# Optimization experiments

Hardware: AMD Instinct MI355X
Metric: run time of the kernel (lower is better)

## Reference

```python
import jax, jax.numpy as jnp
import numpy as np

B, S, D, NH = 8, 2048, 1024, 8
HD = D // NH          # 128 head dim
UP = 2752             # round_up(2.6667*1024, 64) gated FFN up dim
EPS = 1e-6


def setup_inputs() -> dict:
    key = jax.random.key(0)
    ks = jax.random.split(key, 10)
    s_hd = 1.0 / np.sqrt(HD)
    s_d = 1.0 / np.sqrt(D)
    s_up = 1.0 / np.sqrt(UP)
    return {
        "x": jax.random.normal(ks[0], (B, S, D), jnp.float32),
        "rms1_w": 1.0 + 0.1 * jax.random.normal(ks[1], (D,), jnp.float32),
        "rms2_w": 1.0 + 0.1 * jax.random.normal(ks[2], (D,), jnp.float32),
        # block-diagonal per-head input projections for the 4 gates (i,f,z,o)
        "Wg": jax.random.normal(ks[3], (4, NH, HD, HD), jnp.float32) * s_hd,
        # block-diagonal per-head recurrent weights for the 4 gates
        "R": jax.random.normal(ks[4], (4, NH, HD, HD), jnp.float32) * s_hd,
        "b": jax.random.normal(ks[5], (4, D), jnp.float32) * 0.1,
        "gn_w": 1.0 + 0.1 * jax.random.normal(ks[6], (D,), jnp.float32),
        "W_gate": jax.random.normal(ks[7], (D, UP), jnp.float32) * s_d,
        "W_up": jax.random.normal(ks[8], (D, UP), jnp.float32) * s_d,
        "W_down": jax.random.normal(ks[9], (UP, D), jnp.float32) * s_up,
    }


def _rmsnorm(x, w):
    xf = x.astype(jnp.float32)
    return xf * jax.lax.rsqrt(jnp.mean(xf * xf, axis=-1, keepdims=True) + EPS) * w


def _slstm_block(x, rms1_w, rms2_w, Wg, R, b, gn_w, W_gate, W_up, W_down):
    # --- norm + sLSTM layer ---
    xn = _rmsnorm(x, rms1_w)                     # [B,S,D]
    xh = xn.reshape(B, S, NH, HD)
    # precompute input-side gate preactivations for all timesteps: [S,B,4,NH,HD]
    gx = jnp.einsum('bsni,gnoi->sbgno', xh, Wg) + b.reshape(4, NH, HD)

    zeros = jnp.zeros((B, NH, HD), jnp.float32)
    init = (zeros, zeros, zeros, zeros)          # h, c, n, m

    def step(carry, g):
        h, c, n, m = carry
        pre = g + jnp.einsum('bni,gnoi->bgno', h, R)   # [B,4,NH,HD]
        ir, fr, zr, o_r = pre[:, 0], pre[:, 1], pre[:, 2], pre[:, 3]
        logfplusm = m + jax.nn.log_sigmoid(fr)
        mnew = jnp.maximum(ir, logfplusm)
        i = jnp.exp(ir - mnew)
        f = jnp.exp(logfplusm - mnew)
        cnew = f * c + i * jnp.tanh(zr)
        nnew = f * n + i
        hnew = jax.nn.sigmoid(o_r) * cnew / nnew
        return (hnew, cnew, nnew, mnew), hnew

    (hl, cl, nl, ml), hs = jax.lax.scan(step, init, gx)
    hs = jnp.transpose(hs, (1, 0, 2, 3))         # [B,S,NH,HD]
    # per-head group norm (zero-mean layernorm within each head), weight only
    mu = jnp.mean(hs, axis=-1, keepdims=True)
    var = jnp.var(hs, axis=-1, keepdims=True)
    y = ((hs - mu) * jax.lax.rsqrt(var + EPS)).reshape(B, S, D) * gn_w
    x = x + y                                    # residual
    # --- norm + gated SiLU FFN ---
    xn2 = _rmsnorm(x, rms2_w)
    ff = (jax.nn.silu(xn2 @ W_gate) * (xn2 @ W_up)) @ W_down
    out = x + ff
    state = jnp.stack([hl, cl, nl, ml])          # [4,B,NH,HD] last (h,c,n,m)
    return out, state


def reference(x, rms1_w, rms2_w, Wg, R, b, gn_w, W_gate, W_up, W_down):
    return _slstm_block(x, rms1_w, rms2_w, Wg, R, b, gn_w, W_gate, W_up, W_down)
```

## Files before the change

### kernel.cpp

```cpp
#include <hip/hip_runtime.h>

typedef __bf16 bf16;
typedef bf16 bf16x8 __attribute__((ext_vector_type(8)));
typedef bf16 bf16x4 __attribute__((ext_vector_type(4)));
typedef float f32x4 __attribute__((ext_vector_type(4)));

#define B_ 8
#define S_ 2048
#define D_ 1024
#define NH_ 8
#define HD_ 128
#define UPP 2816
#define ROWS (B_*S_)

__device__ __forceinline__ void gload_lds16(const void* gsrc, void* ldsdst) {
  __builtin_amdgcn_global_load_lds(
      (const __attribute__((address_space(1))) void*)gsrc,
      (__attribute__((address_space(3))) void*)ldsdst, 16, 0, 0);
}

__global__ __launch_bounds__(256) void pack_wgr_kernel(
    const float* __restrict__ Wg, const float* __restrict__ R, const float* __restrict__ bv,
    bf16* __restrict__ Wgpk, bf16* __restrict__ Rpk, float* __restrict__ biaspk)
{
  const float K2 = 1.442695040888963f;
  int idx = blockIdx.x * 256 + threadIdx.x;
  if (idx < 8*512*128) {
    int k = idx & 127, j = (idx >> 7) & 511, n = idx >> 16;
    int g = (j >> 4) & 3, o = ((j >> 6) << 4) | (j & 15);
    float sc = (g == 2) ? 2.f*K2 : K2;
    size_t src = (((size_t)(g*8 + n)*128 + o)*128 + k);
    Wgpk[idx] = (bf16)(Wg[src] * sc);
    Rpk[idx]  = (bf16)(R[src] * sc);
  }
  if (idx < 8*512) {
    int j = idx & 511, n = idx >> 9;
    int g = (j >> 4) & 3, o = ((j >> 6) << 4) | (j & 15);
    float sc = (g == 2) ? 2.f*K2 : K2;
    biaspk[idx] = bv[g*1024 + n*128 + o] * sc;
  }
}

__global__ __launch_bounds__(256) void packT_kernel(
    const float* __restrict__ in, bf16* __restrict__ out,
    int K_out, int N_out, int K_in, int N_in)
{
  __shared__ float tile[64][65];
  int k0 = blockIdx.x * 64, j0 = blockIdx.y * 64;
  int tj = threadIdx.x & 63, t4 = threadIdx.x >> 6;
  #pragma unroll
  for (int p = 0; p < 16; ++p) {
    int kk = p*4 + t4, k = k0 + kk, j = j0 + tj;
    tile[kk][tj] = (k < K_in && j < N_in) ? in[(size_t)k * N_in + j] : 0.f;
  }
  __syncthreads();
  #pragma unroll
  for (int p = 0; p < 16; ++p) {
    int jj = p*4 + t4, j = j0 + jj, k = k0 + tj;
    if (j < N_out && k < K_out) out[(size_t)j * K_out + k] = (bf16)tile[tj][jj];
  }
}

__global__ __launch_bounds__(256) void rmsnorm1_kernel(
    const float* __restrict__ x, const float* __restrict__ w, bf16* __restrict__ xn)
{
  const int row = blockIdx.x, t = threadIdx.x;
  const size_t base = (size_t)row * D_;
  float4 xv = ((const float4*)(x + base))[t];
  float p = xv.x*xv.x + xv.y*xv.y + xv.z*xv.z + xv.w*xv.w;
  #pragma unroll
  for (int m = 1; m <= 32; m <<= 1) p += __shfl_xor(p, m);
  __shared__ float red[4];
  if ((t & 63) == 0) red[t >> 6] = p;
  __syncthreads();
  float rs = rsqrtf((red[0]+red[1]+red[2]+red[3]) * (1.f/1024.f) + 1e-6f);
  float4 wv = ((const float4*)w)[t];
  bf16x4 o;
  o[0] = (bf16)(xv.x*rs*wv.x); o[1] = (bf16)(xv.y*rs*wv.y);
  o[2] = (bf16)(xv.z*rs*wv.z); o[3] = (bf16)(xv.w*rs*wv.w);
  ((bf16x4*)(xn + base))[t] = o;
}

#define BM 128
#define BN 128
#define BKK 64
template<int MODE>
__global__ __launch_bounds__(256) void gemm_bt(
    const bf16* __restrict__ A, int lda,
    const bf16* __restrict__ B, int ldb,
    float* Cf, bf16* Cb, int ldc,
    const float* __restrict__ bias, const float* res, const bf16* gatein, int K)
{
  __shared__ __align__(16) bf16 As[BM*BKK];
  __shared__ __align__(16) bf16 Bs[BN*BKK];
  if constexpr (MODE == 0) {
    const int h = blockIdx.z;
    A += h * HD_;
    B += (size_t)h * (512*128);
    Cb += (size_t)h * ((size_t)ROWS * 512);
    bias += h * 512;
  }
  const int tid = threadIdx.x;
  const int lane = tid & 63, wave = tid >> 6;
  const int row0 = blockIdx.y * BM, col0 = blockIdx.x * BN;
  const int srow = lane >> 3, scol = (lane & 7) * 8;
  const int wr = (wave >> 1) * 64, wc = (wave & 1) * 64;
  const int fr = lane & 15, fg = lane >> 4;
  f32x4 acc[4][4] = {};

  for (int k0 = 0; k0 < K; k0 += BKK) {
    __syncthreads();
    #pragma unroll
    for (int c = 0; c < 4; ++c) {
      const int slot = wave * 4 + c;
      const int r = slot * 8 + srow;
      gload_lds16(A + (size_t)(row0 + r) * lda + (k0 + scol), &As[slot * 512]);
      gload_lds16(B + (size_t)(col0 + r) * ldb + (k0 + scol), &Bs[slot * 512]);
    }
    __syncthreads();
    #pragma unroll
    for (int kk = 0; kk < 2; ++kk) {
      bf16x8 af[4], bfv[4];
      #pragma unroll
      for (int m = 0; m < 4; ++m)
        af[m] = *(const bf16x8*)&As[(wr + m*16 + fr)*BKK + kk*32 + fg*8];
      #pragma unroll
      for (int nn = 0; nn < 4; ++nn)
        bfv[nn] = *(const bf16x8*)&Bs[(wc + nn*16 + fr)*BKK + kk*32 + fg*8];
      #pragma unroll
      for (int m = 0; m < 4; ++m)
        #pragma unroll
        for (int nn = 0; nn < 4; ++nn)
          acc[m][nn] = __builtin_amdgcn_mfma_f32_16x16x32_bf16(af[m], bfv[nn], acc[m][nn], 0, 0, 0);
    }
  }

  #pragma unroll
  for (int m = 0; m < 4; ++m) {
    const int rbase = row0 + wr + m*16 + fg*4;
    #pragma unroll
    for (int nn = 0; nn < 4; ++nn) {
      const int col = col0 + wc + nn*16 + fr;
      #pragma unroll
      for (int j = 0; j < 4; ++j) {
        const size_t off = (size_t)(rbase + j) * ldc + col;
        float v = acc[m][nn][j];
        if constexpr (MODE == 0) Cb[off] = (bf16)(v + bias[col]);
        if constexpr (MODE == 1) Cb[off] = (bf16)v;
        if constexpr (MODE == 2) Cf[off] = v + res[off];
        if constexpr (MODE == 3) {
          float gf = (float)gatein[off];
          Cb[off] = (bf16)(gf / (1.f + __expf(-gf)) * v);
        }
      }
    }
  }
}

__global__ __launch_bounds__(512, 1) void recur_kernel(
    const bf16* __restrict__ gx, const bf16* __restrict__ Rpk,
    bf16* __restrict__ hs, float* __restrict__ stateOut)
{
  const int n  = blockIdx.x >> 2;
  const int bp = blockIdx.x & 3;
  const int tid = threadIdx.x, w = tid >> 6, l = tid & 63;
  const int b16 = l & 15, fg = l >> 4;
  const int bl  = l & 1;
  const int r16 = (l >> 1) & 15;
  const int b   = bp*2 + bl;
  const int o   = w*16 + r16;
  const bool act = (l < 32);

  __shared__ __align__(16) bf16 H[2][2][136];
  __shared__ __align__(16) float scr[8][4][2][17];
  for (int i = tid; i < 2*2*136; i += 512) ((bf16*)H)[i] = (bf16)0.f;
  __syncthreads();

  bf16x8 rf[4][4];
  #pragma unroll
  for (int g = 0; g < 4; ++g)
    #pragma unroll
    for (int kk = 0; kk < 4; ++kk)
      rf[g][kk] = *(const bf16x8*)&Rpk[(size_t)n*65536 + (size_t)(w*64 + g*16 + b16)*128 + kk*32 + fg*8];

  f32x4 zv = {0.f, 0.f, 0.f, 0.f};
  asm volatile("" : "+v"(zv));

  float cS = 0.f, nS = 0.f, mS = 0.f, hv = 0.f;

  const bf16* gxp = gx + (size_t)n * ROWS * 512 + (size_t)b * S_ * 512
                    + (size_t)w * 64 + r16;
  bf16* hsp = hs + (size_t)b * S_ * D_ + n * HD_ + o;

  bf16 ga[4][4];
  #pragma unroll
  for (int g = 0; g < 4; ++g) {
    ga[0][g] = gxp[(size_t)0*512 + g*16];
    ga[1][g] = gxp[(size_t)1*512 + g*16];
  }

  auto step = [&](const bf16 (&Hr)[2][136], bf16 (&Hw)[2][136], int s,
                  bf16 (&gU)[4], bf16 (&gF)[4]) {
    bf16x8 hf[4];
    #pragma unroll
    for (int kk = 0; kk < 4; ++kk)
      hf[kk] = *(const bf16x8*)&Hr[b16 & 1][kk*32 + fg*8];

    {
      int sf = (s + 2 < S_) ? s + 2 : 0;
      #pragma unroll
      for (int g = 0; g < 4; ++g)
        gF[g] = gxp[(size_t)sf*512 + g*16];
    }

    f32x4 acc[4];
    #pragma unroll
    for (int g = 0; g < 4; ++g)
      acc[g] = __builtin_amdgcn_mfma_f32_16x16x32_bf16(rf[g][0], hf[0], zv, 0, 0, 0);
    #pragma unroll
    for (int kk = 1; kk < 4; ++kk)
      #pragma unroll
      for (int g = 0; g < 4; ++g)
        acc[g] = __builtin_amdgcn_mfma_f32_16x16x32_bf16(rf[g][kk], hf[kk], acc[g], 0, 0, 0);

    if (b16 < 2) {
      #pragma unroll
      for (int g = 0; g < 4; ++g)
        *(f32x4*)&scr[w][g][b16][fg*4] = acc[g];
    }
    float pre[4];
    #pragma unroll
    for (int g = 0; g < 4; ++g)
      pre[g] = scr[w][g][bl][r16];

    float ir  = pre[0] + (float)gU[0];
    float fr_ = pre[1] + (float)gU[1];
    float zr  = pre[2] + (float)gU[2];
    float og  = pre[3] + (float)gU[3];
    float t   = __builtin_amdgcn_exp2f(-fr_);
    float lfm = mS - __builtin_amdgcn_logf(1.f + t);
    float d   = ir - lfm;
    float e   = __builtin_amdgcn_exp2f(-fabsf(d));
    float iG  = (d >= 0.f) ? 1.f : e;
    float fG  = (d >= 0.f) ? e : 1.f;
    mS = fmaxf(ir, lfm);
    float e2  = __builtin_amdgcn_exp2f(zr);
    float th  = 1.f - 2.f*__builtin_amdgcn_rcpf(e2 + 1.f);
    cS = fG*cS + iG*th;
    nS = fG*nS + iG;
    float eo  = __builtin_amdgcn_exp2f(-og);
    hv = cS * __builtin_amdgcn_rcpf(nS + nS*eo);

    bf16 hb = (bf16)hv;
    if (act) {
      Hw[bl][o] = hb;
      hsp[(size_t)s*D_] = hb;
    }

    __builtin_amdgcn_sched_barrier(0);
    __builtin_amdgcn_s_waitcnt(0xC07F);
    __builtin_amdgcn_s_barrier();
    __builtin_amdgcn_sched_barrier(0);
  };

  for (int s = 0; s < S_; s += 4) {
    step(H[0], H[1], s,     ga[0], ga[2]);
    step(H[1], H[0], s + 1, ga[1], ga[3]);
    step(H[0], H[1], s + 2, ga[2], ga[0]);
    step(H[1], H[0], s + 3, ga[3], ga[1]);
  }

  if (act) {
    const float LN2 = 0.6931471805599453f;
    size_t sb = ((size_t)b*NH_ + n)*HD_ + o;
    stateOut[sb]         = hv;
    stateOut[8192  + sb] = cS;
    stateOut[16384 + sb] = nS;
    stateOut[24576 + sb] = mS * LN2;
  }
}

__global__ __launch_bounds__(256) void fuse_gn_kernel(
    const bf16* __restrict__ hs, const float* __restrict__ x,
    const float* __restrict__ gnw, const float* __restrict__ r2w,
    float* __restrict__ xr, bf16* __restrict__ xn2)
{
  const int row = blockIdx.x, t = threadIdx.x;
  const size_t base = (size_t)row * D_;
  bf16x4 hraw = ((const bf16x4*)(hs + base))[t];
  float h0 = (float)hraw[0], h1 = (float)hraw[1], h2 = (float)hraw[2], h3 = (float)hraw[3];
  float4 xv = ((const float4*)(x + base))[t];
  float sum = h0 + h1 + h2 + h3;
  float sq  = h0*h0 + h1*h1 + h2*h2 + h3*h3;
  #pragma unroll
  for (int m = 1; m <= 16; m <<= 1) { sum += __shfl_xor(sum, m); sq += __shfl_xor(sq, m); }
  float mu = sum * (1.f/128.f);
  float var = sq * (1.f/128.f) - mu*mu;
  float rstd = rsqrtf(var + 1e-6f);
  float4 gw = ((const float4*)gnw)[t];
  float r0 = xv.x + (h0-mu)*rstd*gw.x;
  float r1 = xv.y + (h1-mu)*rstd*gw.y;
  float r2 = xv.z + (h2-mu)*rstd*gw.z;
  float r3 = xv.w + (h3-mu)*rstd*gw.w;
  ((float4*)(xr + base))[t] = make_float4(r0, r1, r2, r3);
  float p = r0*r0 + r1*r1 + r2*r2 + r3*r3;
  #pragma unroll
  for (int m = 1; m <= 32; m <<= 1) p += __shfl_xor(p, m);
  __shared__ float red[4];
  if ((t & 63) == 0) red[t >> 6] = p;
  __syncthreads();
  float rs = rsqrtf((red[0]+red[1]+red[2]+red[3]) * (1.f/1024.f) + 1e-6f);
  float4 w2 = ((const float4*)r2w)[t];
  bf16x4 o;
  o[0] = (bf16)(r0*rs*w2.x); o[1] = (bf16)(r1*rs*w2.y);
  o[2] = (bf16)(r2*rs*w2.z); o[3] = (bf16)(r3*rs*w2.w);
  ((bf16x4*)(xn2 + base))[t] = o;
}

extern "C" void kernel_launch(void* const* d_in, const int* in_sizes, int n_in,
                              void* d_out, int out_size, void* d_ws, size_t ws_size,
                              hipStream_t stream)
{
  const float* x     = (const float*)d_in[0];
  const float* rms1w = (const float*)d_in[1];
  const float* rms2w = (const float*)d_in[2];
  const float* Wg    = (const float*)d_in[3];
  const float* R     = (const float*)d_in[4];
  const float* bvec  = (const float*)d_in[5];
  const float* gnw   = (const float*)d_in[6];
  const float* Wgate = (const float*)d_in[7];
  const float* Wup   = (const float*)d_in[8];
  const float* Wdown = (const float*)d_in[9];
  float* out = (float*)d_out;
  float* stateOut = out + (size_t)ROWS * D_;

  char* ws = (char*)d_ws;
  size_t off = 0;
  auto alloc = [&](size_t bytes) -> void* {
    void* p = ws + off; off += (bytes + 255) & ~(size_t)255; return p;
  };
  bf16*  xn     = (bf16*)alloc((size_t)ROWS * D_ * 2);
  bf16*  hsbuf  = (bf16*)alloc((size_t)ROWS * D_ * 2);
  bf16*  bigbuf = (bf16*)alloc((size_t)NH_ * ROWS * 512 * 2);
  bf16*  Wgpk   = (bf16*)alloc(8*512*128*2);
  bf16*  Rpk    = (bf16*)alloc(8*512*128*2);
  float* biaspk = (float*)alloc(8*512*4);
  bf16*  Wgatepk = (bf16*)alloc((size_t)UPP * D_ * 2);
  bf16*  Wuppk   = (bf16*)alloc((size_t)UPP * D_ * 2);
  bf16*  Wdownpk = (bf16*)alloc((size_t)D_ * UPP * 2);

  pack_wgr_kernel<<<2048, 256, 0, stream>>>(Wg, R, bvec, Wgpk, Rpk, biaspk);
  packT_kernel<<<dim3(16, 44), 256, 0, stream>>>(Wgate, Wgatepk, 1024, 2816, 1024, 2752);
  packT_kernel<<<dim3(16, 44), 256, 0, stream>>>(Wup,   Wuppk,   1024, 2816, 1024, 2752);
  packT_kernel<<<dim3(44, 16), 256, 0, stream>>>(Wdown, Wdownpk, 2816, 1024, 2752, 1024);

  rmsnorm1_kernel<<<ROWS, 256, 0, stream>>>(x, rms1w, xn);

  gemm_bt<0><<<dim3(4, 128, 8), 256, 0, stream>>>(xn, D_, Wgpk, 128,
      nullptr, bigbuf, 512, biaspk, nullptr, nullptr, 128);

  recur_kernel<<<32, 512, 0, stream>>>(bigbuf, Rpk, hsbuf, stateOut);

  fuse_gn_kernel<<<ROWS, 256, 0, stream>>>(hsbuf, x, gnw, rms2w, out, xn);

  bf16* gate = bigbuf;
  gemm_bt<1><<<dim3(22, 128), 256, 0, stream>>>(xn, D_, Wgatepk, D_,
      nullptr, gate, UPP, nullptr, nullptr, nullptr, D_);
  gemm_bt<3><<<dim3(22, 128), 256, 0, stream>>>(xn, D_, Wuppk, D_,
      nullptr, gate, UPP, nullptr, nullptr, gate, D_);

  gemm_bt<2><<<dim3(8, 128), 256, 0, stream>>>(gate, UPP, Wdownpk, UPP,
      out, nullptr, D_, nullptr, out, nullptr, UPP);
}
```

Measured before the change: 2.029 ms.

## Compute sLSTM gate math directly from MFMA accumulators, dropping LDS scratch shuffle

The recurrent kernel no longer writes MFMA accumulators to an LDS scratch buffer and reads them back redistributed across 32 lanes. Instead the 8 lanes holding batch columns 0-1 each process 4 output rows directly from their accumulator registers, with vectorized bf16x4 gate loads, H writes and state stores. This removes an LDS round trip from the serial per-timestep critical path. The trade-off is that the transcendental work is concentrated on fewer lanes, 4 elements each, which lengthens the per-lane ALU chain.

```diff
diff --git a/kernel.cpp b/kernel.cpp
--- a/kernel.cpp
+++ b/kernel.cpp
@@ -165,14 +165,11 @@
   const int bp = blockIdx.x & 3;
   const int tid = threadIdx.x, w = tid >> 6, l = tid & 63;
   const int b16 = l & 15, fg = l >> 4;
-  const int bl  = l & 1;
-  const int r16 = (l >> 1) & 15;
-  const int b   = bp*2 + bl;
-  const int o   = w*16 + r16;
-  const bool act = (l < 32);
+  const bool act = (b16 < 2);
+  const int b   = bp*2 + b16;
+  const int o0  = w*16 + fg*4;
 
   __shared__ __align__(16) bf16 H[2][2][136];
-  __shared__ __align__(16) float scr[8][4][2][17];
   for (int i = tid; i < 2*2*136; i += 512) ((bf16*)H)[i] = (bf16)0.f;
   __syncthreads();
 
@@ -186,31 +183,33 @@
   f32x4 zv = {0.f, 0.f, 0.f, 0.f};
   asm volatile("" : "+v"(zv));
 
-  float cS = 0.f, nS = 0.f, mS = 0.f, hv = 0.f;
+  float cS[4] = {}, nS[4] = {}, mS[4] = {}, hv[4] = {};
 
   const bf16* gxp = gx + (size_t)n * ROWS * 512 + (size_t)b * S_ * 512
-                    + (size_t)w * 64 + r16;
-  bf16* hsp = hs + (size_t)b * S_ * D_ + n * HD_ + o;
-
-  bf16 ga[4][4];
-  #pragma unroll
-  for (int g = 0; g < 4; ++g) {
-    ga[0][g] = gxp[(size_t)0*512 + g*16];
-    ga[1][g] = gxp[(size_t)1*512 + g*16];
+                    + (size_t)w * 64 + fg*4;
+  bf16* hsp = hs + (size_t)b * S_ * D_ + n * HD_ + o0;
+
+  bf16x4 ga[4][4];
+  if (act) {
+    #pragma unroll
+    for (int g = 0; g < 4; ++g) {
+      ga[0][g] = *(const bf16x4*)(gxp + (size_t)0*512 + g*16);
+      ga[1][g] = *(const bf16x4*)(gxp + (size_t)1*512 + g*16);
+    }
   }
 
   auto step = [&](const bf16 (&Hr)[2][136], bf16 (&Hw)[2][136], int s,
-                  bf16 (&gU)[4], bf16 (&gF)[4]) {
+                  bf16x4 (&gU)[4], bf16x4 (&gF)[4]) {
     bf16x8 hf[4];
     #pragma unroll
     for (int kk = 0; kk < 4; ++kk)
       hf[kk] = *(const bf16x8*)&Hr[b16 & 1][kk*32 + fg*8];
 
-    {
+    if (act) {
       int sf = (s + 2 < S_) ? s + 2 : 0;
       #pragma unroll
       for (int g = 0; g < 4; ++g)
-        gF[g] = gxp[(size_t)sf*512 + g*16];
+        gF[g] = *(const bf16x4*)(gxp + (size_t)sf*512 + g*16);
     }
 
     f32x4 acc[4];
@@ -223,38 +222,31 @@
       for (int g = 0; g < 4; ++g)
         acc[g] = __builtin_amdgcn_mfma_f32_16x16x32_bf16(rf[g][kk], hf[kk], acc[g], 0, 0, 0);
 
-    if (b16 < 2) {
-      #pragma unroll
-      for (int g = 0; g < 4; ++g)
-        *(f32x4*)&scr[w][g][b16][fg*4] = acc[g];
-    }
-    float pre[4];
-    #pragma unroll
-    for (int g = 0; g < 4; ++g)
-      pre[g] = scr[w][g][bl][r16];
-
-    float ir  = pre[0] + (float)gU[0];
-    float fr_ = pre[1] + (float)gU[1];
-    float zr  = pre[2] + (float)gU[2];
-    float og  = pre[3] + (float)gU[3];
-    float t   = __builtin_amdgcn_exp2f(-fr_);
-    float lfm = mS - __builtin_amdgcn_logf(1.f + t);
-    float d   = ir - lfm;
-    float e   = __builtin_amdgcn_exp2f(-fabsf(d));
-    float iG  = (d >= 0.f) ? 1.f : e;
-    float fG  = (d >= 0.f) ? e : 1.f;
-    mS = fmaxf(ir, lfm);
-    float e2  = __builtin_amdgcn_exp2f(zr);
-    float th  = 1.f - 2.f*__builtin_amdgcn_rcpf(e2 + 1.f);
-    cS = fG*cS + iG*th;
-    nS = fG*nS + iG;
-    float eo  = __builtin_amdgcn_exp2f(-og);
-    hv = cS * __builtin_amdgcn_rcpf(nS + nS*eo);
-
-    bf16 hb = (bf16)hv;
     if (act) {
-      Hw[bl][o] = hb;
-      hsp[(size_t)s*D_] = hb;
+      bf16x4 hb;
+      #pragma unroll
+      for (int jj = 0; jj < 4; ++jj) {
+        float ir  = acc[0][jj] + (float)gU[0][jj];
+        float fr_ = acc[1][jj] + (float)gU[1][jj];
+        float zr  = acc[2][jj] + (float)gU[2][jj];
+        float og  = acc[3][jj] + (float)gU[3][jj];
+        float t   = __builtin_amdgcn_exp2f(-fr_);
+        float lfm = mS[jj] - __builtin_amdgcn_logf(1.f + t);
+        float d   = ir - lfm;
+        float e   = __builtin_amdgcn_exp2f(-fabsf(d));
+        float iG  = (d >= 0.f) ? 1.f : e;
+        float fG  = (d >= 0.f) ? e : 1.f;
+        mS[jj] = fmaxf(ir, lfm);
+        float e2  = __builtin_amdgcn_exp2f(zr);
+        float th  = 1.f - 2.f*__builtin_amdgcn_rcpf(e2 + 1.f);
+        cS[jj] = fG*cS[jj] + iG*th;
+        nS[jj] = fG*nS[jj] + iG;
+        float eo  = __builtin_amdgcn_exp2f(-og);
+        hv[jj] = cS[jj] * __builtin_amdgcn_rcpf(nS[jj] + nS[jj]*eo);
+        hb[jj] = (bf16)hv[jj];
+      }
+      *(bf16x4*)&Hw[b16][o0] = hb;
+      *(bf16x4*)(hsp + (size_t)s*D_) = hb;
     }
 
     __builtin_amdgcn_sched_barrier(0);
@@ -272,11 +264,11 @@
 
   if (act) {
     const float LN2 = 0.6931471805599453f;
-    size_t sb = ((size_t)b*NH_ + n)*HD_ + o;
-    stateOut[sb]         = hv;
-    stateOut[8192  + sb] = cS;
-    stateOut[16384 + sb] = nS;
-    stateOut[24576 + sb] = mS * LN2;
+    size_t sb = ((size_t)b*NH_ + n)*HD_ + o0;
+    *(float4*)(stateOut +         sb) = make_float4(hv[0], hv[1], hv[2], hv[3]);
+    *(float4*)(stateOut +  8192 + sb) = make_float4(cS[0], cS[1], cS[2], cS[3]);
+    *(float4*)(stateOut + 16384 + sb) = make_float4(nS[0], nS[1], nS[2], nS[3]);
+    *(float4*)(stateOut + 24576 + sb) = make_float4(mS[0]*LN2, mS[1]*LN2, mS[2]*LN2, mS[3]*LN2);
   }
 }
 
```

Result: slower. 4.411 ms (+117.4%).
